# Optimization experiments

Measured on AMD Instinct MI355X. Metric: run time of the kernel, lower is better.

The kernel has to match this reference:

```python
import jax, jax.numpy as jnp
import numpy as np
import math

K = 8       # wavelet order (k)
C = 8       # channels (c)
ALPHA = 64  # retained Fourier modes
L = 0       # coarsest level
B = 32
N = 8192    # power of two


def setup_inputs() -> dict:
    key = jax.random.key(0)
    ks = jax.random.split(key, 14)
    ck = C * K
    scale = 1.0 / (ck * ck)  # matches torch: 1/(c*k)**2
    f32 = jnp.float32
    inp = {
        "x": jax.random.normal(ks[0], (B, N, C, K), dtype=f32),
        # SparseKernelFT1d weights (complex, stored as re/im): scale * rand
        "wA_re": scale * jax.random.uniform(ks[1], (ck, ck, ALPHA), dtype=f32),
        "wA_im": scale * jax.random.uniform(ks[2], (ck, ck, ALPHA), dtype=f32),
        "wB_re": scale * jax.random.uniform(ks[3], (ck, ck, ALPHA), dtype=f32),
        "wB_im": scale * jax.random.uniform(ks[4], (ck, ck, ALPHA), dtype=f32),
        "wC_re": scale * jax.random.uniform(ks[5], (ck, ck, ALPHA), dtype=f32),
        "wC_im": scale * jax.random.uniform(ks[6], (ck, ck, ALPHA), dtype=f32),
        # T0 linear layer (k -> k)
        "T0_w": jax.random.normal(ks[7], (K, K), dtype=f32) / math.sqrt(K),
        "T0_b": 0.01 * jax.random.normal(ks[8], (K,), dtype=f32),
        # Legendre wavelet filter buffers: ec_* are [H0.T;H1.T] / [G0.T;G1.T] (2k,k),
        # rc_* are [H0;G0] / [H1;G1] (2k,k). Stand-ins: random orthonormal-ish matrices
        # scaled like wavelet filters (same math regardless of exact values).
        "ec_s": jax.random.normal(ks[9], (2 * K, K), dtype=f32) / math.sqrt(2 * K),
        "ec_d": jax.random.normal(ks[10], (2 * K, K), dtype=f32) / math.sqrt(2 * K),
        "rc_e": jax.random.normal(ks[11], (2 * K, K), dtype=f32) / math.sqrt(2 * K),
        "rc_o": jax.random.normal(ks[12], (2 * K, K), dtype=f32) / math.sqrt(2 * K),
    }
    return inp


def _sparse_ft(x, w_re, w_im):
    # x: [B, N, c, k] -> spectral mixing over first ALPHA rfft modes
    Bb, Nn, c, k = x.shape
    xv = x.reshape(Bb, Nn, c * k).transpose(0, 2, 1)   # [B, ck, N]
    xf = jnp.fft.rfft(xv)                               # [B, ck, N//2+1] complex
    l = min(ALPHA, Nn // 2 + 1)
    W = (w_re[:, :, :l] + 1j * w_im[:, :, :l]).astype(jnp.complex64)
    of = jnp.einsum('bix,iox->box', xf[:, :, :l], W)
    out_ft = jnp.zeros((Bb, c * k, Nn // 2 + 1), dtype=jnp.complex64).at[:, :, :l].set(of)
    xo = jnp.fft.irfft(out_ft, n=Nn)                    # [B, ck, N] real
    return xo.transpose(0, 2, 1).reshape(Bb, Nn, c, k)


def reference(x, wA_re, wA_im, wB_re, wB_im, wC_re, wC_im, T0_w, T0_b,
              ec_s, ec_d, rc_e, rc_o):
    Bb, Nn, c, k = x.shape
    ns = int(math.floor(math.log2(Nn)))
    Ud, Us = [], []
    # --- decomposition ---
    for _ in range(ns - L):
        xa = jnp.concatenate([x[:, ::2], x[:, 1::2]], axis=-1)  # [B, N/2, c, 2k]
        d = xa @ ec_d                                           # [B, N/2, c, k]
        s = xa @ ec_s
        Ud.append(_sparse_ft(d, wA_re, wA_im) + _sparse_ft(s, wB_re, wB_im))
        Us.append(_sparse_ft(d, wC_re, wC_im))
        x = s
    # --- coarsest-level linear ---
    x = x @ T0_w.T + T0_b
    # --- reconstruction (u_s is None branch) ---
    for i in range(ns - 1 - L, -1, -1):
        x = x + Us[i]
        xc = jnp.concatenate([x, Ud[i]], axis=-1)               # [B, n, c, 2k]
        x_e = xc @ rc_e
        x_o = xc @ rc_o
        Bc, Nc, cc, _ = xc.shape
        x = jnp.stack([x_e, x_o], axis=2).reshape(Bc, Nc * 2, cc, K)  # interleave even/odd
    return (x,) + tuple(Ud) + tuple(Us)
```

## Files before the change

### kernel.cpp

```cpp
#include <hip/hip_runtime.h>

#define BB 32
#define CKD 64
#define CC 8
#define KK 8
#define FPW 132

__device__ const int D_FCB[14] = {0,32,48,56,60,62,63,64,65,66,67,68,69,70};
__device__ const int D_TB[14] = {0,64,96,112,120,124,126,127,128,129,130,131,132,133};
__device__ const int D_LS[14] = {0,64,128,192,256,320,384,417,434,443,448,451,453,454};
__device__ const int D_L[13]  = {64,64,64,64,64,64,33,17,9,5,3,2,1};
__device__ const int D_FTOF[13] = {0,524288,786432,917504,983040,1015808,1032192,
                                   1048576,1064960,1081344,1097728,1114112,1130496};

typedef __attribute__((ext_vector_type(4))) short s4v;
typedef __attribute__((ext_vector_type(8))) short s8v;
typedef __attribute__((ext_vector_type(4))) float f4v;

static __device__ __forceinline__ float4 ld4(const float* p){ return *(const float4*)p; }
static __device__ __forceinline__ size_t d_udo(int i){ return 33554432ull - (16777216u >> i); }
static __device__ __forceinline__ size_t d_uso(int i){ return 50329600ull - (16777216u >> i); }
static __device__ __forceinline__ size_t d_tof(int i){ return 128ull * (8192u - (8192u >> i)); }

static __device__ __forceinline__ unsigned short b16(float f) {
    unsigned u = __float_as_uint(f);
    u += 0x7FFFu + ((u >> 16) & 1u);
    return (unsigned short)(u >> 16);
}
static __device__ __forceinline__ float fb16(unsigned short h) {
    return __uint_as_float(((unsigned)h) << 16);
}

__global__ __launch_bounds__(256) void gen_tbl2_k(unsigned short* __restrict__ Th,
        unsigned short* __restrict__ Tl, unsigned short* __restrict__ Tfh,
        unsigned short* __restrict__ Tfl) {
    int lvl = blockIdx.y;
    int nh = 4096 >> lvl;
    int idx = blockIdx.x * 256 + threadIdx.x;
    if (blockIdx.z == 0) {
        if (idx >= nh * 128) return;
        int t = idx >> 7, k = idx & 127, x = k >> 1;
        int l = nh / 2 + 1; if (l > 64) l = 64;
        float v = 0.f;
        if (x < l) {
            int r = (x * t) & (nh - 1);
            float th = 6.283185307179586f * ((float)r / (float)nh);
            float s, c; sincosf(th, &s, &c);
            v = (k & 1) ? s : c;
        }
        unsigned short hi = b16(v);
        unsigned short lo = b16(v - fb16(hi));
        size_t off = d_tof(lvl) + idx;
        Th[off] = hi; Tl[off] = lo;
    } else {
        int nhp = nh < 128 ? 128 : nh;
        if (idx >= 128 * nhp) return;
        int j = idx & 7;
        int lane = (idx >> 3) & 63;
        int mt = (idx >> 9) & 7;
        int kb = idx >> 12;
        int row = mt*16 + (lane & 15);
        int t = kb*32 + (lane >> 4)*8 + j;
        int x = row >> 1;
        int l = nh / 2 + 1; if (l > 64) l = 64;
        float v = 0.f;
        if (x < l && t < nh) {
            int r = (x * t) & (nh - 1);
            float th = 6.283185307179586f * ((float)r / (float)nh);
            float s, c; sincosf(th, &s, &c);
            v = (row & 1) ? -s : c;
        }
        unsigned short hi = b16(v);
        unsigned short lo = b16(v - fb16(hi));
        size_t off = (size_t)D_FTOF[lvl] + idx;
        Tfh[off] = hi; Tfl[off] = lo;
    }
}

__global__ __launch_bounds__(256) void decomp_k(const float* __restrict__ xin,
        const float* __restrict__ ecd, const float* __restrict__ ecs,
        float* __restrict__ dslot, float* __restrict__ sslot, int nh) {
    int idx = blockIdx.x * 256 + threadIdx.x;
    if (idx >= BB * nh * CC) return;
    int c = idx & 7;
    int t = (idx >> 3) % nh;
    int b = idx / (nh * CC);
    const float* p0 = xin + ((size_t)b * 2 * nh + 2 * t) * CKD + c * KK;
    float xa[16];
    float4 v;
    v = ld4(p0);      xa[0]=v.x; xa[1]=v.y; xa[2]=v.z; xa[3]=v.w;
    v = ld4(p0+4);    xa[4]=v.x; xa[5]=v.y; xa[6]=v.z; xa[7]=v.w;
    v = ld4(p0+64);   xa[8]=v.x; xa[9]=v.y; xa[10]=v.z; xa[11]=v.w;
    v = ld4(p0+68);   xa[12]=v.x; xa[13]=v.y; xa[14]=v.z; xa[15]=v.w;
    float dd[8], ss[8];
    #pragma unroll
    for (int m = 0; m < 8; m++) { dd[m] = 0.f; ss[m] = 0.f; }
    #pragma unroll
    for (int j = 0; j < 16; j++) {
        float xv = xa[j];
        #pragma unroll
        for (int m = 0; m < 8; m++) {
            dd[m] = fmaf(xv, ecd[j*8+m], dd[m]);
            ss[m] = fmaf(xv, ecs[j*8+m], ss[m]);
        }
    }
    size_t ob = ((size_t)b * nh + t) * CKD + c * KK;
    *(float4*)(dslot+ob)   = make_float4(dd[0],dd[1],dd[2],dd[3]);
    *(float4*)(dslot+ob+4) = make_float4(dd[4],dd[5],dd[6],dd[7]);
    *(float4*)(sslot+ob)   = make_float4(ss[0],ss[1],ss[2],ss[3]);
    *(float4*)(sslot+ob+4) = make_float4(ss[4],ss[5],ss[6],ss[7]);
}

__global__ __launch_bounds__(256) void decomp_small_k(const float* __restrict__ s4base,
        const float* __restrict__ ecd, const float* __restrict__ ecs,
        const float* __restrict__ T0w, const float* __restrict__ T0b,
        float* __restrict__ outbuf, float* __restrict__ xt0) {
    __shared__ float sA[128*64];
    __shared__ float sB[64*64];
    int b = blockIdx.x, tid = threadIdx.x;
    for (int lvl = 5; lvl <= 12; lvl++) {
        int nh = 4096 >> lvl;
        const float* src = (lvl == 5) ? (s4base + (size_t)b*256*CKD)
                                      : (((lvl - 6) & 1) ? sB : sA);
        float* dst = ((lvl - 5) & 1) ? sB : sA;
        float* dG = outbuf + d_udo(lvl) + (size_t)b*nh*CKD;
        float* sG = outbuf + d_uso(lvl) + (size_t)b*nh*CKD;
        for (int q = tid; q < nh*8; q += 256) {
            int c = q & 7, t = q >> 3;
            const float* p0 = src + (size_t)(2*t)*CKD + c*KK;
            float xa[16];
            float4 v;
            v = ld4(p0);      xa[0]=v.x; xa[1]=v.y; xa[2]=v.z; xa[3]=v.w;
            v = ld4(p0+4);    xa[4]=v.x; xa[5]=v.y; xa[6]=v.z; xa[7]=v.w;
            v = ld4(p0+64);   xa[8]=v.x; xa[9]=v.y; xa[10]=v.z; xa[11]=v.w;
            v = ld4(p0+68);   xa[12]=v.x; xa[13]=v.y; xa[14]=v.z; xa[15]=v.w;
            float dd[8], ss[8];
            #pragma unroll
            for (int m = 0; m < 8; m++) { dd[m] = 0.f; ss[m] = 0.f; }
            #pragma unroll
            for (int j = 0; j < 16; j++) {
                float xv = xa[j];
                #pragma unroll
                for (int m = 0; m < 8; m++) {
                    dd[m] = fmaf(xv, ecd[j*8+m], dd[m]);
                    ss[m] = fmaf(xv, ecs[j*8+m], ss[m]);
                }
            }
            size_t ob = (size_t)t * CKD + c * KK;
            *(float4*)(dG+ob)   = make_float4(dd[0],dd[1],dd[2],dd[3]);
            *(float4*)(dG+ob+4) = make_float4(dd[4],dd[5],dd[6],dd[7]);
            *(float4*)(sG+ob)   = make_float4(ss[0],ss[1],ss[2],ss[3]);
            *(float4*)(sG+ob+4) = make_float4(ss[4],ss[5],ss[6],ss[7]);
            float* dl = dst + t*CKD + c*KK;
            #pragma unroll
            for (int j = 0; j < 8; j++) dl[j] = ss[j];
        }
        __syncthreads();
    }
    if (tid < 64) {
        int m = tid & 7, c = tid >> 3;
        const float* xr = sB + c*KK;
        float a = T0b[m];
        #pragma unroll
        for (int j = 0; j < 8; j++) a = fmaf(xr[j], T0w[m*8+j], a);
        xt0[(size_t)b*64 + tid] = a;
    }
}

__global__ __launch_bounds__(256) void fft_fwd_mfma_k(const float* __restrict__ outbuf,
        const unsigned short* __restrict__ Tfh, const unsigned short* __restrict__ Tfl,
        float* __restrict__ xfpf, float2* __restrict__ xf_all) {
    __shared__ unsigned vp[128*FPW];
    int slot = blockIdx.x;
    int lvl = 0;
    while (lvl < 12 && slot >= D_FCB[lvl+1]) lvl++;
    int nh = 4096 >> lvl;
    int ch = D_FCB[lvl+1] - D_FCB[lvl];
    int t0s = (slot - D_FCB[lvl]) * 128;
    int b = blockIdx.y;
    const float* V0 = outbuf + d_udo(lvl) + (size_t)b * nh * CKD;
    const float* V1 = outbuf + d_uso(lvl) + (size_t)b * nh * CKD;
    const unsigned short* THb = Tfh + D_FTOF[lvl];
    const unsigned short* TLb = Tfl + D_FTOF[lvl];
    int tid = threadIdx.x;
    int w = tid >> 6, lane = tid & 63;
    int col = lane & 15, khi = lane >> 4;
    int mt0 = w * 2;
    #pragma unroll
    for (int q = 0; q < 16; q++) {
        int fi = tid + 256*q;
        int tl_ = fi >> 5;
        int t = t0s + tl_;
        int iq = fi & 31;
        int z = iq >> 4;
        int i4 = (iq & 15) * 4;
        const float* Vz = z ? V1 : V0;
        float4 v = make_float4(0.f,0.f,0.f,0.f);
        if (t < nh) v = ld4(Vz + (size_t)t*CKD + i4);
        const float* pv = &v.x;
        int rowb = z*64 + i4;
        #pragma unroll
        for (int j = 0; j < 4; j++) {
            int row = rowb + j;
            float f = pv[j];
            unsigned u = __float_as_uint(f);
            unsigned hi = u & 0xFFFF0000u;
            float r = f - __uint_as_float(hi);
            unsigned lo = __float_as_uint(r) & 0xFFFF0000u;
            int cw = tl_ ^ (((row >> 3) & 7) << 2);
            vp[row*FPW + cw] = (hi >> 16) | lo;
        }
    }
    __syncthreads();
    int rrow[8], rswz[8];
    #pragma unroll
    for (int n = 0; n < 8; n++) {
        rrow[n] = n*16 + col;
        rswz[n] = ((rrow[n] >> 3) & 7) << 2;
    }
    f4v acc[2][8];
    #pragma unroll
    for (int m = 0; m < 2; m++)
        #pragma unroll
        for (int n = 0; n < 8; n++) acc[m][n] = (f4v){0.f,0.f,0.f,0.f};
    int kb0 = (slot - D_FCB[lvl]) * 4;
    #pragma unroll
    for (int kk = 0; kk < 4; kk++) {
        int kb = kb0 + kk;
        s8v ah[2], al[2];
        #pragma unroll
        for (int m = 0; m < 2; m++) {
            size_t fo = (((size_t)kb*8 + (mt0 + m))*64 + lane)*8;
            ah[m] = *(const s8v*)(THb + fo);
            al[m] = *(const s8v*)(TLb + fo);
        }
        int cb = kk*32 + khi*8;
        #pragma unroll
        for (int n = 0; n < 8; n++) {
            const unsigned* pr = vp + rrow[n]*FPW;
            uint4 w0 = *(const uint4*)(pr + (cb ^ rswz[n]));
            uint4 w1 = *(const uint4*)(pr + ((cb + 4) ^ rswz[n]));
            s8v bh, bl;
            const unsigned* pw = &w0.x;
            #pragma unroll
            for (int j = 0; j < 4; j++) {
                bh[j] = (short)(pw[j] & 0xFFFFu);
                bl[j] = (short)(pw[j] >> 16);
            }
            pw = &w1.x;
            #pragma unroll
            for (int j = 0; j < 4; j++) {
                bh[4+j] = (short)(pw[j] & 0xFFFFu);
                bl[4+j] = (short)(pw[j] >> 16);
            }
            #pragma unroll
            for (int m = 0; m < 2; m++) {
                acc[m][n] = __builtin_amdgcn_mfma_f32_16x16x32_bf16(ah[m], bh, acc[m][n], 0,0,0);
                acc[m][n] = __builtin_amdgcn_mfma_f32_16x16x32_bf16(ah[m], bl, acc[m][n], 0,0,0);
                acc[m][n] = __builtin_amdgcn_mfma_f32_16x16x32_bf16(al[m], bh, acc[m][n], 0,0,0);
            }
        }
    }
    if (ch == 1) {
        float* XB = (float*)xf_all + (size_t)lvl*524288 + (size_t)b*16384;
        #pragma unroll
        for (int m = 0; m < 2; m++) {
            int m0 = (mt0 + m)*16 + khi*4;
            #pragma unroll
            for (int n = 0; n < 8; n++) {
                int ic = n*16 + col;
                int z = ic >> 6, i = ic & 63;
                float* X = XB + (size_t)z*8192;
                #pragma unroll
                for (int r = 0; r < 4; r++) {
                    int row = m0 + r;
                    X[(((size_t)(row >> 1)*64 + i) << 1) | (row & 1)] = acc[m][n][r];
                }
            }
        }
    } else {
        #pragma unroll
        for (int m = 0; m < 2; m++) {
            int m0 = (mt0 + m)*16 + khi*4;
            #pragma unroll
            for (int n = 0; n < 8; n++) {
                int ic = n*16 + col;
                int z = ic >> 6, i = ic & 63;
                float* P = xfpf + ((size_t)slot*64 + (size_t)b*2 + z) * 8192;
                #pragma unroll
                for (int r = 0; r < 4; r++)
                    P[(size_t)(m0 + r)*64 + i] = acc[m][n][r];
            }
        }
    }
}

__global__ __launch_bounds__(256) void reduce_fwd_k(const float* __restrict__ xfpf,
        float2* __restrict__ xf_all) {
    int lvl = blockIdx.y;
    int e = blockIdx.x * 256 + threadIdx.x;
    int j = e & 4095;
    int bz = e >> 12;
    int x = j >> 6, i = j & 63;
    int c0 = D_FCB[lvl], c1 = D_FCB[lvl+1];
    float re = 0.f, im = 0.f;
    for (int c = c0; c < c1; c++) {
        size_t base = ((size_t)c*64 + bz) * 8192;
        re += xfpf[base + (size_t)(2*x)*64 + i];
        im += xfpf[base + (size_t)(2*x+1)*64 + i];
    }
    xf_all[(size_t)lvl*262144 + (size_t)bz*4096 + j] = make_float2(re, im);
}

__global__ __launch_bounds__(256) void mix_all_k(const float2* __restrict__ xf_all,
        const float* __restrict__ wAr, const float* __restrict__ wAi,
        const float* __restrict__ wBr, const float* __restrict__ wBi,
        const float* __restrict__ wCr, const float* __restrict__ wCi,
        unsigned short* __restrict__ ofh, unsigned short* __restrict__ ofl) {
    int lvl = 0;
    while (lvl < 12 && (int)blockIdx.x >= D_LS[lvl+1]) lvl++;
    int x = blockIdx.x - D_LS[lvl];
    int nh = 4096 >> lvl;
    const float2* xfL = xf_all + (size_t)lvl*262144;
    int tid = threadIdx.x;
    int o = tid & 63, wq = tid >> 6;
    __shared__ float2 sxd[BB*CKD];
    __shared__ float2 sxs[BB*CKD];
    __shared__ float  swt[6][16*CKD];
    for (int q = tid; q < BB*CKD; q += 256) {
        int b = q >> 6, i = q & 63;
        sxd[q] = xfL[((size_t)b*2 + 0)*4096 + x*64 + i];
        sxs[q] = xfL[((size_t)b*2 + 1)*4096 + x*64 + i];
    }
    float2 aud[8], aus[8];
    #pragma unroll
    for (int j=0;j<8;j++){ aud[j]=make_float2(0.f,0.f); aus[j]=make_float2(0.f,0.f); }
    for (int ic = 0; ic < 4; ic++) {
        __syncthreads();
        for (int q = tid; q < 16*CKD; q += 256) {
            int ii = q >> 6, oo = q & 63;
            size_t a = ((size_t)(ic*16+ii)*64 + oo)*64 + x;
            swt[0][q] = wAr[a]; swt[1][q] = wAi[a];
            swt[2][q] = wBr[a]; swt[3][q] = wBi[a];
            swt[4][q] = wCr[a]; swt[5][q] = wCi[a];
        }
        __syncthreads();
        #pragma unroll 4
        for (int ii = 0; ii < 16; ii++) {
            float ar = swt[0][ii*64+o], ai_ = swt[1][ii*64+o];
            float br = swt[2][ii*64+o], bi_ = swt[3][ii*64+o];
            float cr = swt[4][ii*64+o], ci_ = swt[5][ii*64+o];
            int i = ic*16 + ii;
            #pragma unroll
            for (int j = 0; j < 8; j++) {
                float2 xd = sxd[(wq*8+j)*64 + i];
                float2 xs = sxs[(wq*8+j)*64 + i];
                aud[j].x += xd.x*ar - xd.y*ai_ + xs.x*br - xs.y*bi_;
                aud[j].y += xd.x*ai_ + xd.y*ar + xs.x*bi_ + xs.y*br;
                aus[j].x += xd.x*cr - xd.y*ci_;
                aus[j].y += xd.x*ci_ + xd.y*cr;
            }
        }
    }
    float w = (x == 0 || 2*x == nh) ? 1.f : 2.f;
    float sc = w / (float)nh;
    int k0 = 2*x;
    #pragma unroll
    for (int j = 0; j < 8; j++) {
        int b = wq*8 + j;
        {
            size_t base = (((size_t)lvl*32 + b)*2 + 0)*8192;
            float A = sc*aud[j].x, Bn = -sc*aud[j].y;
            unsigned short ha = b16(A),  hb = b16(Bn);
            unsigned short la = b16(A - fb16(ha)), lb = b16(Bn - fb16(hb));
            ofh[base + (size_t)k0*64 + o]     = ha;
            ofh[base + (size_t)(k0+1)*64 + o] = hb;
            ofl[base + (size_t)k0*64 + o]     = la;
            ofl[base + (size_t)(k0+1)*64 + o] = lb;
        }
        {
            size_t base = (((size_t)lvl*32 + b)*2 + 1)*8192;
            float A = sc*aus[j].x, Bn = -sc*aus[j].y;
            unsigned short ha = b16(A),  hb = b16(Bn);
            unsigned short la = b16(A - fb16(ha)), lb = b16(Bn - fb16(hb));
            ofh[base + (size_t)k0*64 + o]     = ha;
            ofh[base + (size_t)(k0+1)*64 + o] = hb;
            ofl[base + (size_t)k0*64 + o]     = la;
            ofl[base + (size_t)(k0+1)*64 + o] = lb;
        }
    }
}

__global__ __launch_bounds__(256) void fft_inv_mfma_k(
        const unsigned short* __restrict__ ofh, const unsigned short* __restrict__ ofl,
        const unsigned short* __restrict__ Th,  const unsigned short* __restrict__ Tl,
        float* __restrict__ outbuf) {
    __shared__ unsigned short gh[2*64*132];
    __shared__ unsigned short gl[2*64*132];
    int lvl = 0;
    while (lvl < 12 && (int)blockIdx.x >= D_TB[lvl+1]) lvl++;
    int g = blockIdx.x - D_TB[lvl];
    int nh = 4096 >> lvl;
    int tbase = g * 64;
    int b = blockIdx.y;
    int tid = threadIdx.x;
    #pragma unroll
    for (int q = 0; q < 8; q++) {
        int fi = tid + 256*q;
        int z = fi >> 10;
        int r = fi & 1023;
        int k = r & 127, oct = r >> 7;
        const unsigned short* Gh = ofh + (((size_t)lvl*32 + b)*2 + z)*8192;
        const unsigned short* Gl = ofl + (((size_t)lvl*32 + b)*2 + z)*8192;
        uint4 vh = *(const uint4*)(Gh + (size_t)k*64 + oct*8);
        uint4 vl = *(const uint4*)(Gl + (size_t)k*64 + oct*8);
        const unsigned* ph = &vh.x;
        const unsigned* pl = &vl.x;
        #pragma unroll
        for (int i = 0; i < 8; i++) {
            unsigned wd = ph[i>>1];
            gh[z*8448 + (oct*8+i)*132 + k] = (i&1) ? (unsigned short)(wd>>16) : (unsigned short)(wd&0xFFFF);
            wd = pl[i>>1];
            gl[z*8448 + (oct*8+i)*132 + k] = (i&1) ? (unsigned short)(wd>>16) : (unsigned short)(wd&0xFFFF);
        }
    }
    __syncthreads();
    int w = tid >> 6;
    int lane = tid & 63;
    int tb = tbase + w*16;
    if (tb >= nh) return;
    int trow = lane & 15, khi = lane >> 4;
    int tA = tb + trow; if (tA >= nh) tA = nh - 1;
    const unsigned short* THp = Th + d_tof(lvl) + (size_t)tA*128 + khi*8;
    const unsigned short* TLp = Tl + d_tof(lvl) + (size_t)tA*128 + khi*8;
    f4v acc[8];
    #pragma unroll
    for (int n = 0; n < 8; n++) acc[n] = (f4v){0.f,0.f,0.f,0.f};
    #pragma unroll
    for (int kk = 0; kk < 4; kk++) {
        s8v ah = *(const s8v*)(THp + kk*32);
        s8v al = *(const s8v*)(TLp + kk*32);
        #pragma unroll
        for (int n = 0; n < 8; n++) {
            int z = n >> 2;
            int off = z*8448 + ((n & 3)*16 + trow)*132 + kk*32 + khi*8;
            s4v b0 = *(const s4v*)(gh + off);
            s4v b1 = *(const s4v*)(gh + off + 4);
            s4v c0 = *(const s4v*)(gl + off);
            s4v c1 = *(const s4v*)(gl + off + 4);
            s8v bh = __builtin_shufflevector(b0, b1, 0,1,2,3,4,5,6,7);
            s8v bl = __builtin_shufflevector(c0, c1, 0,1,2,3,4,5,6,7);
            acc[n] = __builtin_amdgcn_mfma_f32_16x16x32_bf16(ah, bh, acc[n], 0, 0, 0);
            acc[n] = __builtin_amdgcn_mfma_f32_16x16x32_bf16(ah, bl, acc[n], 0, 0, 0);
            acc[n] = __builtin_amdgcn_mfma_f32_16x16x32_bf16(al, bh, acc[n], 0, 0, 0);
        }
    }
    float* U0 = outbuf + d_udo(lvl) + (size_t)b * nh * CKD;
    float* U1 = outbuf + d_uso(lvl) + (size_t)b * nh * CKD;
    int thi4 = khi * 4;
    #pragma unroll
    for (int n = 0; n < 8; n++) {
        float* U = (n >> 2) ? U1 : U0;
        int ocol = (n & 3)*16 + trow;
        #pragma unroll
        for (int r = 0; r < 4; r++) {
            int t = tb + thi4 + r;
            if (t < nh) U[(size_t)t*64 + ocol] = acc[n][r];
        }
    }
}

__global__ __launch_bounds__(256) void recon_small_k(const float* __restrict__ xt0,
        const float* __restrict__ outbuf,
        const float* __restrict__ rce, const float* __restrict__ rco,
        float* __restrict__ rb0) {
    __shared__ float xA[128*64];
    __shared__ float xB[64*64];
    int b = blockIdx.x, tid = threadIdx.x;
    if (tid < 64) xB[tid] = xt0[(size_t)b*64 + tid];
    __syncthreads();
    for (int i = 12; i >= 6; i--) {
        int nh = 4096 >> i;
        const float* cur = ((i == 12) || !(i & 1)) ? xB : xA;
        float* nxt = (i & 1) ? xB : xA;
        const float* Us = outbuf + d_uso(i) + (size_t)b*nh*CKD;
        const float* Ud = outbuf + d_udo(i) + (size_t)b*nh*CKD;
        for (int q = tid; q < nh*8; q += 256) {
            int c = q & 7, t = q >> 3;
            size_t base = (size_t)t*CKD + c*KK;
            float xc[16];
            float4 a0 = ld4(cur+base), a1 = ld4(cur+base+4);
            float4 u0 = ld4(Us+base),  u1 = ld4(Us+base+4);
            float4 d0 = ld4(Ud+base),  d1 = ld4(Ud+base+4);
            xc[0]=a0.x+u0.x; xc[1]=a0.y+u0.y; xc[2]=a0.z+u0.z; xc[3]=a0.w+u0.w;
            xc[4]=a1.x+u1.x; xc[5]=a1.y+u1.y; xc[6]=a1.z+u1.z; xc[7]=a1.w+u1.w;
            xc[8]=d0.x;  xc[9]=d0.y;  xc[10]=d0.z; xc[11]=d0.w;
            xc[12]=d1.x; xc[13]=d1.y; xc[14]=d1.z; xc[15]=d1.w;
            float e[8], o2[8];
            #pragma unroll
            for (int m = 0; m < 8; m++) { e[m] = 0.f; o2[m] = 0.f; }
            #pragma unroll
            for (int j = 0; j < 16; j++) {
                float xv = xc[j];
                #pragma unroll
                for (int m = 0; m < 8; m++) {
                    e[m]  = fmaf(xv, rce[j*8+m], e[m]);
                    o2[m] = fmaf(xv, rco[j*8+m], o2[m]);
                }
            }
            if (i > 6) {
                float* pe = nxt + (size_t)(2*t)*CKD + c*KK;
                #pragma unroll
                for (int j = 0; j < 8; j++) { pe[j] = e[j]; pe[CKD + j] = o2[j]; }
            } else {
                float* pe = rb0 + ((size_t)b*128 + 2*t)*CKD + c*KK;
                *(float4*)(pe)      = make_float4(e[0],e[1],e[2],e[3]);
                *(float4*)(pe+4)    = make_float4(e[4],e[5],e[6],e[7]);
                *(float4*)(pe+64)   = make_float4(o2[0],o2[1],o2[2],o2[3]);
                *(float4*)(pe+68)   = make_float4(o2[4],o2[5],o2[6],o2[7]);
            }
        }
        __syncthreads();
    }
}

__global__ __launch_bounds__(256) void recon_k(const float* __restrict__ xin,
        const float* __restrict__ us, const float* __restrict__ ud,
        const float* __restrict__ rce, const float* __restrict__ rco,
        float* __restrict__ xout, int nh) {
    int idx = blockIdx.x*256 + threadIdx.x;
    if (idx >= BB*nh*CC) return;
    int c = idx & 7;
    int t = (idx >> 3) % nh;
    int b = idx / (nh*CC);
    size_t base = ((size_t)b*nh + t)*CKD + c*KK;
    float xc[16];
    float4 a0 = ld4(xin+base), a1 = ld4(xin+base+4);
    float4 u0 = ld4(us+base),  u1 = ld4(us+base+4);
    float4 d0 = ld4(ud+base),  d1 = ld4(ud+base+4);
    xc[0]=a0.x+u0.x; xc[1]=a0.y+u0.y; xc[2]=a0.z+u0.z; xc[3]=a0.w+u0.w;
    xc[4]=a1.x+u1.x; xc[5]=a1.y+u1.y; xc[6]=a1.z+u1.z; xc[7]=a1.w+u1.w;
    xc[8]=d0.x;  xc[9]=d0.y;  xc[10]=d0.z; xc[11]=d0.w;
    xc[12]=d1.x; xc[13]=d1.y; xc[14]=d1.z; xc[15]=d1.w;
    float e[8], o2[8];
    #pragma unroll
    for (int m = 0; m < 8; m++) { e[m] = 0.f; o2[m] = 0.f; }
    #pragma unroll
    for (int j = 0; j < 16; j++) {
        float xv = xc[j];
        #pragma unroll
        for (int m = 0; m < 8; m++) {
            e[m]  = fmaf(xv, rce[j*8+m], e[m]);
            o2[m] = fmaf(xv, rco[j*8+m], o2[m]);
        }
    }
    size_t ob = ((size_t)b*2*nh + 2*t)*CKD + c*KK;
    *(float4*)(xout+ob)      = make_float4(e[0],e[1],e[2],e[3]);
    *(float4*)(xout+ob+4)    = make_float4(e[4],e[5],e[6],e[7]);
    *(float4*)(xout+ob+64)   = make_float4(o2[0],o2[1],o2[2],o2[3]);
    *(float4*)(xout+ob+68)   = make_float4(o2[4],o2[5],o2[6],o2[7]);
}

extern "C" void kernel_launch(void* const* d_in, const int* in_sizes, int n_in,
                              void* d_out, int out_size, void* d_ws, size_t ws_size,
                              hipStream_t stream) {
    const float* x   = (const float*)d_in[0];
    const float* wAr = (const float*)d_in[1];
    const float* wAi = (const float*)d_in[2];
    const float* wBr = (const float*)d_in[3];
    const float* wBi = (const float*)d_in[4];
    const float* wCr = (const float*)d_in[5];
    const float* wCi = (const float*)d_in[6];
    const float* T0w = (const float*)d_in[7];
    const float* T0b = (const float*)d_in[8];
    const float* ecs = (const float*)d_in[9];
    const float* ecd = (const float*)d_in[10];
    const float* rce = (const float*)d_in[11];
    const float* rco = (const float*)d_in[12];
    float* out = (float*)d_out;
    float* wsf = (float*)d_ws;

    size_t p = 0;
    float2* xf_all = (float2*)(wsf + p); p += 6815744;
    unsigned short* ofh = (unsigned short*)(wsf + p); p += 3407872;
    unsigned short* ofl = (unsigned short*)(wsf + p); p += 3407872;
    unsigned short* Th  = (unsigned short*)(wsf + p); p += 528384;
    unsigned short* Tl  = (unsigned short*)(wsf + p); p += 528384;
    unsigned short* Tfh = (unsigned short*)(wsf + p); p += 573440;
    unsigned short* Tfl = (unsigned short*)(wsf + p); p += 573440;
    float*  xt0  = wsf + p; p += 2048;
    float*  rb0  = wsf + p; p += 4194304;
    float*  rb1  = wsf + p; p += 8388608;
    float*  xfpf = wsf + p; p += 36700160;
    (void)ws_size; (void)in_sizes; (void)n_in; (void)out_size;

    size_t udo[13], uso[13];
    for (int i = 0; i < 13; i++) {
        udo[i] = 33554432ull - (16777216u >> i);
        uso[i] = 50329600ull - (16777216u >> i);
    }

    gen_tbl2_k<<<dim3(2048, 13, 2), 256, 0, stream>>>(Th, Tl, Tfh, Tfl);

    for (int i = 0; i < 5; i++) {
        int nh = 4096 >> i;
        const float* xin_l = (i == 0) ? x : (out + uso[i-1]);
        int tot = BB * nh * CC;
        decomp_k<<<(tot + 255)/256, 256, 0, stream>>>(xin_l, ecd, ecs, out + udo[i], out + uso[i], nh);
    }
    decomp_small_k<<<BB, 256, 0, stream>>>(out + uso[4], ecd, ecs, T0w, T0b, out, xt0);

    fft_fwd_mfma_k<<<dim3(70, BB), 256, 0, stream>>>(out, Tfh, Tfl, xfpf, xf_all);
    reduce_fwd_k<<<dim3(1024, 5), 256, 0, stream>>>(xfpf, xf_all);
    mix_all_k<<<454, 256, 0, stream>>>(xf_all, wAr, wAi, wBr, wBi, wCr, wCi, ofh, ofl);
    fft_inv_mfma_k<<<dim3(133, BB), 256, 0, stream>>>(ofh, ofl, Th, Tl, out);

    recon_small_k<<<BB, 256, 0, stream>>>(xt0, out, rce, rco, rb0);
    const float* rin = rb0;
    for (int i = 5; i >= 0; i--) {
        int nh = 4096 >> i;
        float* ro = (i == 0) ? out : ((i & 1) ? rb1 : rb0);
        int tot = BB * nh * CC;
        recon_k<<<(tot + 255)/256, 256, 0, stream>>>(rin, out + uso[i], out + udo[i], rce, rco, ro, nh);
        rin = ro;
    }
}
```

Baseline: 481.0 us.

## Pre-transpose spectral weights and reorder mix blocks by mode with 512 threads

Adds a kernel that transposes the six complex weight arrays so each Fourier mode's 64x64 block is contiguous, replacing the stride-64 gather in the mixing kernel with coalesced loads. The mixing kernel now orders blocks mode-major, so the levels sharing a mode run next to each other and can reuse that mode's weights from cache. Block size doubles to 512 with half the batch rows per thread, which raises parallelism per block. The extra transpose launch and workspace buffer add some cost each call.

```diff
diff --git a/kernel.cpp b/kernel.cpp
--- a/kernel.cpp
+++ b/kernel.cpp
@@ -8,10 +8,13 @@
 
 __device__ const int D_FCB[14] = {0,32,48,56,60,62,63,64,65,66,67,68,69,70};
 __device__ const int D_TB[14] = {0,64,96,112,120,124,126,127,128,129,130,131,132,133};
-__device__ const int D_LS[14] = {0,64,128,192,256,320,384,417,434,443,448,451,453,454};
 __device__ const int D_L[13]  = {64,64,64,64,64,64,33,17,9,5,3,2,1};
 __device__ const int D_FTOF[13] = {0,524288,786432,917504,983040,1015808,1032192,
                                    1048576,1064960,1081344,1097728,1114112,1130496};
+__device__ const int D_XP[65] = {0,13,25,36,46,56,65,74,83,92,100,108,116,124,132,140,
+    148,156,163,170,177,184,191,198,205,212,219,226,233,240,247,254,261,268,274,280,
+    286,292,298,304,310,316,322,328,334,340,346,352,358,364,370,376,382,388,394,400,
+    406,412,418,424,430,436,442,448,454};
 
 typedef __attribute__((ext_vector_type(4))) short s4v;
 typedef __attribute__((ext_vector_type(8))) short s8v;
@@ -75,6 +78,25 @@
         size_t off = (size_t)D_FTOF[lvl] + idx;
         Tfh[off] = hi; Tfl[off] = lo;
     }
+}
+
+__global__ __launch_bounds__(256) void wtr_k(const float* __restrict__ wAr,
+        const float* __restrict__ wAi, const float* __restrict__ wBr,
+        const float* __restrict__ wBi, const float* __restrict__ wCr,
+        const float* __restrict__ wCi, float* __restrict__ wt) {
+    int x = blockIdx.x, arr = blockIdx.y;
+    const float* W;
+    switch (arr) {
+        case 0: W = wAr; break;
+        case 1: W = wAi; break;
+        case 2: W = wBr; break;
+        case 3: W = wBi; break;
+        case 4: W = wCr; break;
+        default: W = wCi; break;
+    }
+    float* o = wt + ((size_t)arr*64 + x)*4096;
+    for (int q = threadIdx.x; q < 4096; q += 256)
+        o[q] = W[(size_t)q*64 + x];
 }
 
 __global__ __launch_bounds__(256) void decomp_k(const float* __restrict__ xin,
@@ -312,14 +334,12 @@
     xf_all[(size_t)lvl*262144 + (size_t)bz*4096 + j] = make_float2(re, im);
 }
 
-__global__ __launch_bounds__(256) void mix_all_k(const float2* __restrict__ xf_all,
-        const float* __restrict__ wAr, const float* __restrict__ wAi,
-        const float* __restrict__ wBr, const float* __restrict__ wBi,
-        const float* __restrict__ wCr, const float* __restrict__ wCi,
+__global__ __launch_bounds__(512) void mix_all_k(const float2* __restrict__ xf_all,
+        const float* __restrict__ wt,
         unsigned short* __restrict__ ofh, unsigned short* __restrict__ ofl) {
-    int lvl = 0;
-    while (lvl < 12 && (int)blockIdx.x >= D_LS[lvl+1]) lvl++;
-    int x = blockIdx.x - D_LS[lvl];
+    int x = 0;
+    while (x < 64 && (int)blockIdx.x >= D_XP[x+1]) x++;
+    int lvl = blockIdx.x - D_XP[x];
     int nh = 4096 >> lvl;
     const float2* xfL = xf_all + (size_t)lvl*262144;
     int tid = threadIdx.x;
@@ -327,22 +347,20 @@
     __shared__ float2 sxd[BB*CKD];
     __shared__ float2 sxs[BB*CKD];
     __shared__ float  swt[6][16*CKD];
-    for (int q = tid; q < BB*CKD; q += 256) {
+    for (int q = tid; q < BB*CKD; q += 512) {
         int b = q >> 6, i = q & 63;
         sxd[q] = xfL[((size_t)b*2 + 0)*4096 + x*64 + i];
         sxs[q] = xfL[((size_t)b*2 + 1)*4096 + x*64 + i];
     }
-    float2 aud[8], aus[8];
-    #pragma unroll
-    for (int j=0;j<8;j++){ aud[j]=make_float2(0.f,0.f); aus[j]=make_float2(0.f,0.f); }
+    float2 aud[4], aus[4];
+    #pragma unroll
+    for (int j=0;j<4;j++){ aud[j]=make_float2(0.f,0.f); aus[j]=make_float2(0.f,0.f); }
+    const float* WTx = wt + (size_t)x*4096;
     for (int ic = 0; ic < 4; ic++) {
         __syncthreads();
-        for (int q = tid; q < 16*CKD; q += 256) {
-            int ii = q >> 6, oo = q & 63;
-            size_t a = ((size_t)(ic*16+ii)*64 + oo)*64 + x;
-            swt[0][q] = wAr[a]; swt[1][q] = wAi[a];
-            swt[2][q] = wBr[a]; swt[3][q] = wBi[a];
-            swt[4][q] = wCr[a]; swt[5][q] = wCi[a];
+        for (int q = tid; q < 6*1024; q += 512) {
+            int arr = q >> 10, r = q & 1023;
+            swt[arr][r] = WTx[(size_t)arr*262144 + ic*1024 + r];
         }
         __syncthreads();
         #pragma unroll 4
@@ -352,9 +370,9 @@
             float cr = swt[4][ii*64+o], ci_ = swt[5][ii*64+o];
             int i = ic*16 + ii;
             #pragma unroll
-            for (int j = 0; j < 8; j++) {
-                float2 xd = sxd[(wq*8+j)*64 + i];
-                float2 xs = sxs[(wq*8+j)*64 + i];
+            for (int j = 0; j < 4; j++) {
+                float2 xd = sxd[(wq*4+j)*64 + i];
+                float2 xs = sxs[(wq*4+j)*64 + i];
                 aud[j].x += xd.x*ar - xd.y*ai_ + xs.x*br - xs.y*bi_;
                 aud[j].y += xd.x*ai_ + xd.y*ar + xs.x*bi_ + xs.y*br;
                 aus[j].x += xd.x*cr - xd.y*ci_;
@@ -366,8 +384,8 @@
     float sc = w / (float)nh;
     int k0 = 2*x;
     #pragma unroll
-    for (int j = 0; j < 8; j++) {
-        int b = wq*8 + j;
+    for (int j = 0; j < 4; j++) {
+        int b = wq*4 + j;
         {
             size_t base = (((size_t)lvl*32 + b)*2 + 0)*8192;
             float A = sc*aud[j].x, Bn = -sc*aud[j].y;
@@ -588,6 +606,7 @@
     unsigned short* Tl  = (unsigned short*)(wsf + p); p += 528384;
     unsigned short* Tfh = (unsigned short*)(wsf + p); p += 573440;
     unsigned short* Tfl = (unsigned short*)(wsf + p); p += 573440;
+    float*  wt   = wsf + p; p += 1572864;
     float*  xt0  = wsf + p; p += 2048;
     float*  rb0  = wsf + p; p += 4194304;
     float*  rb1  = wsf + p; p += 8388608;
@@ -601,6 +620,7 @@
     }
 
     gen_tbl2_k<<<dim3(2048, 13, 2), 256, 0, stream>>>(Th, Tl, Tfh, Tfl);
+    wtr_k<<<dim3(64, 6), 256, 0, stream>>>(wAr, wAi, wBr, wBi, wCr, wCi, wt);
 
     for (int i = 0; i < 5; i++) {
         int nh = 4096 >> i;
@@ -612,7 +632,7 @@
 
     fft_fwd_mfma_k<<<dim3(70, BB), 256, 0, stream>>>(out, Tfh, Tfl, xfpf, xf_all);
     reduce_fwd_k<<<dim3(1024, 5), 256, 0, stream>>>(xfpf, xf_all);
-    mix_all_k<<<454, 256, 0, stream>>>(xf_all, wAr, wAi, wBr, wBi, wCr, wCi, ofh, ofl);
+    mix_all_k<<<454, 512, 0, stream>>>(xf_all, wt, ofh, ofl);
     fft_inv_mfma_k<<<dim3(133, BB), 256, 0, stream>>>(ofh, ofl, Th, Tl, out);
 
     recon_small_k<<<BB, 256, 0, stream>>>(xt0, out, rce, rco, rb0);
```

Result: no change. 477.1 us (-0.8%).
